# Optimization experiments

Measured on AMD Instinct MI355X. Metric: run time of the kernel, lower is better.

The kernel has to match this reference:

```python
import jax, jax.numpy as jnp
import numpy as np

GROUP = 128          # GPTQ quantization group size
H = 2048             # hidden_size
I = 1408             # moe_intermediate_size
T = 16384            # routed tokens


def _pack_rows(v):
    # v: [in, out] int4 values -> [in//8, out] int32 (8 nibbles per int32 along input dim)
    v = v.reshape(v.shape[0] // 8, 8, v.shape[1]).astype(jnp.int32)
    sh = (4 * jnp.arange(8, dtype=jnp.int32))[None, :, None]
    return (v << sh).sum(axis=1).astype(jnp.int32)


def _pack_cols(v):
    # v: [groups, out] int4 values -> [groups, out//8] int32
    v = v.reshape(v.shape[0], v.shape[1] // 8, 8).astype(jnp.int32)
    sh = (4 * jnp.arange(8, dtype=jnp.int32))[None, None, :]
    return (v << sh).sum(axis=-1).astype(jnp.int32)


def _unpack_rows(qw):
    # [in//8, out] int32 -> [in, out] int4 values
    sh = 4 * jnp.arange(8, dtype=jnp.int32)
    v = (qw[:, None, :] >> sh[None, :, None]) & 0xF
    return v.reshape(qw.shape[0] * 8, qw.shape[1])


def _unpack_cols(qz):
    # [groups, out//8] int32 -> [groups, out] int4 values
    sh = 4 * jnp.arange(8, dtype=jnp.int32)
    v = (qz[:, :, None] >> sh[None, None, :]) & 0xF
    return v.reshape(qz.shape[0], qz.shape[1] * 8)


def _dequant(qw, qz, sc):
    # GPTQ dequant: W[k, n] = (q[k, n] - (zero[g(k), n] + 1)) * scale[g(k), n]
    w = _unpack_rows(qw).astype(sc.dtype)                      # [in, out]
    z = (_unpack_cols(qz) + 1).astype(sc.dtype)                # [groups, out]
    scale = jnp.repeat(sc, GROUP, axis=0)                      # [in, out]
    zero = jnp.repeat(z, GROUP, axis=0)                        # [in, out]
    return (w - zero) * scale


def setup_inputs() -> dict:
    key = jax.random.key(0)
    ks = jax.random.split(key, 10)
    x = jax.random.normal(ks[0], (T, H), dtype=jnp.float32)

    def make_quant(kq, kz, ksc, n_in, n_out):
        q = jax.random.randint(kq, (n_in, n_out), 0, 16, dtype=jnp.int32)
        z = jax.random.randint(kz, (n_in // GROUP, n_out), 0, 15, dtype=jnp.int32)
        sc = jax.random.uniform(ksc, (n_in // GROUP, n_out), dtype=jnp.float32,
                                minval=1e-3, maxval=2e-2)
        return _pack_rows(q), _pack_cols(z), sc

    qw_g, qz_g, sc_g = make_quant(ks[1], ks[2], ks[3], H, I)
    qw_u, qz_u, sc_u = make_quant(ks[4], ks[5], ks[6], H, I)
    qw_d, qz_d, sc_d = make_quant(ks[7], ks[8], ks[9], I, H)
    return {"x": x,
            "qw_gate": qw_g, "qz_gate": qz_g, "sc_gate": sc_g,
            "qw_up": qw_u, "qz_up": qz_u, "sc_up": sc_u,
            "qw_down": qw_d, "qz_down": qz_d, "sc_down": sc_d}


def reference(x, qw_gate, qz_gate, sc_gate, qw_up, qz_up, sc_up,
              qw_down, qz_down, sc_down):
    Wg = _dequant(qw_gate, qz_gate, sc_gate)   # [H, I]
    Wu = _dequant(qw_up, qz_up, sc_up)         # [H, I]
    Wd = _dequant(qw_down, qz_down, sc_down)   # [I, H]
    # fused_gate_up: silu(x @ Wg) * (x @ Wu)
    h = jax.nn.silu(x @ Wg) * (x @ Wu)         # [T, I]
    return h @ Wd                              # [T, H]
```

## Files before the change

kernel.cpp:

```cpp
#include <hip/hip_runtime.h>

#define T_DIM 16384
#define H_DIM 2048
#define I_DIM 1408

typedef _Float16 half8 __attribute__((ext_vector_type(8)));
typedef float floatx4 __attribute__((ext_vector_type(4)));

static_assert(T_DIM % 128 == 0 && H_DIM % 128 == 0 && I_DIM % 128 == 0, "tile divisibility");

__device__ __forceinline__ void async_cp16(const _Float16* gp, _Float16* lp) {
    __builtin_amdgcn_global_load_lds(
        (const __attribute__((address_space(1))) unsigned int*)gp,
        (__attribute__((address_space(3))) unsigned int*)lp,
        16, 0, 0);
}

__global__ void cvt_fp16_kernel(const float* __restrict__ x, _Float16* __restrict__ xh) {
    int i = (blockIdx.x * 256 + threadIdx.x) * 8;
    const float4* p = (const float4*)(x + i);
    float4 a = p[0];
    float4 b = p[1];
    half8 o = { (_Float16)a.x, (_Float16)a.y, (_Float16)a.z, (_Float16)a.w,
                (_Float16)b.x, (_Float16)b.y, (_Float16)b.z, (_Float16)b.w };
    *(half8*)(xh + i) = o;
}

__global__ void dequant_kernel(const int* __restrict__ qw, const int* __restrict__ qz,
                               const float* __restrict__ sc, _Float16* __restrict__ Wt,
                               int K, int N) {
    int kp = blockIdx.x * 64 + threadIdx.x;
    int n  = blockIdx.y;
    if (kp >= (K >> 3)) return;
    int q = qw[kp * N + n];
    int g = kp >> 4;
    float scale = sc[g * N + n];
    int zq = (qz[g * (N >> 3) + (n >> 3)] >> (4 * (n & 7))) & 0xF;
    float zf = (float)(zq + 1);
    half8 o;
#pragma unroll
    for (int j = 0; j < 8; ++j) {
        float w = ((float)((q >> (4 * j)) & 0xF) - zf) * scale;
        o[j] = (_Float16)w;
    }
    *(half8*)(Wt + n * K + kp * 8) = o;
}

__launch_bounds__(256, 2)
__global__ void gemm_gateup_kernel(const _Float16* __restrict__ xh,
                                   const _Float16* __restrict__ Wg,
                                   const _Float16* __restrict__ Wu,
                                   _Float16* __restrict__ h) {
    __shared__ _Float16 As[128 * 32];
    __shared__ _Float16 Bgs[128 * 32];
    __shared__ _Float16 Bus[128 * 32];

    const int tid  = threadIdx.x;
    const int wave = tid >> 6;
    const int lane = tid & 63;
    const int m0 = blockIdx.y * 128;
    const int n0 = blockIdx.x * 128;
    const int wm = wave >> 1;
    const int wn = wave & 1;

    const int r0 = wave * 32 + (lane >> 2);
    const int ke = (lane & 3) * 8;
    const _Float16* agp0 = xh + (m0 + r0) * H_DIM + ke;
    const _Float16* agp1 = agp0 + 16 * H_DIM;
    const _Float16* bgp0 = Wg + (n0 + r0) * H_DIM + ke;
    const _Float16* bgp1 = bgp0 + 16 * H_DIM;
    const _Float16* bup0 = Wu + (n0 + r0) * H_DIM + ke;
    const _Float16* bup1 = bup0 + 16 * H_DIM;
    _Float16* lA0  = As  + wave * 1024;
    _Float16* lA1  = As  + wave * 1024 + 512;
    _Float16* lBg0 = Bgs + wave * 1024;
    _Float16* lBg1 = Bgs + wave * 1024 + 512;
    _Float16* lBu0 = Bus + wave * 1024;
    _Float16* lBu1 = Bus + wave * 1024 + 512;

    const int q4  = lane >> 4;
    const int l15 = lane & 15;
    const int a_base = (wm * 64 + l15) * 32 + q4 * 8;
    const int b_base = (wn * 64 + l15) * 32 + q4 * 8;

    floatx4 zero = {0.f, 0.f, 0.f, 0.f};
    floatx4 accg[4][4], accu[4][4];
#pragma unroll
    for (int mi = 0; mi < 4; ++mi)
#pragma unroll
        for (int ni = 0; ni < 4; ++ni) { accg[mi][ni] = zero; accu[mi][ni] = zero; }

    for (int kt = 0; kt < H_DIM; kt += 32) {
        __syncthreads();
        async_cp16(agp0 + kt, lA0);
        async_cp16(agp1 + kt, lA1);
        async_cp16(bgp0 + kt, lBg0);
        async_cp16(bgp1 + kt, lBg1);
        async_cp16(bup0 + kt, lBu0);
        async_cp16(bup1 + kt, lBu1);
        __syncthreads();

        half8 af[4], bgf[4], buf_[4];
#pragma unroll
        for (int mi = 0; mi < 4; ++mi)
            af[mi] = *(const half8*)(As + a_base + mi * 512);
#pragma unroll
        for (int ni = 0; ni < 4; ++ni) {
            bgf[ni]  = *(const half8*)(Bgs + b_base + ni * 512);
            buf_[ni] = *(const half8*)(Bus + b_base + ni * 512);
        }
#pragma unroll
        for (int mi = 0; mi < 4; ++mi)
#pragma unroll
            for (int ni = 0; ni < 4; ++ni) {
                accg[mi][ni] = __builtin_amdgcn_mfma_f32_16x16x32_f16(af[mi], bgf[ni], accg[mi][ni], 0, 0, 0);
                accu[mi][ni] = __builtin_amdgcn_mfma_f32_16x16x32_f16(af[mi], buf_[ni], accu[mi][ni], 0, 0, 0);
            }
    }

    const int rq = q4 * 4;
#pragma unroll
    for (int mi = 0; mi < 4; ++mi)
#pragma unroll
        for (int ni = 0; ni < 4; ++ni)
#pragma unroll
            for (int r = 0; r < 4; ++r) {
                int row = m0 + wm * 64 + mi * 16 + rq + r;
                int col = n0 + wn * 64 + ni * 16 + l15;
                float g = accg[mi][ni][r];
                float u = accu[mi][ni][r];
                float s = (g / (1.0f + __expf(-g))) * u;
                h[row * I_DIM + col] = (_Float16)s;
            }
}

__launch_bounds__(256, 2)
__global__ void gemm_down_kernel(const _Float16* __restrict__ hh,
                                 const _Float16* __restrict__ Wd,
                                 float* __restrict__ out) {
    __shared__ _Float16 As[128 * 32];
    __shared__ _Float16 Bs[128 * 32];

    const int tid  = threadIdx.x;
    const int wave = tid >> 6;
    const int lane = tid & 63;
    const int m0 = blockIdx.y * 128;
    const int n0 = blockIdx.x * 128;
    const int wm = wave >> 1;
    const int wn = wave & 1;

    const int r0 = wave * 32 + (lane >> 2);
    const int ke = (lane & 3) * 8;
    const _Float16* agp0 = hh + (m0 + r0) * I_DIM + ke;
    const _Float16* agp1 = agp0 + 16 * I_DIM;
    const _Float16* bgp0 = Wd + (n0 + r0) * I_DIM + ke;
    const _Float16* bgp1 = bgp0 + 16 * I_DIM;
    _Float16* lA0 = As + wave * 1024;
    _Float16* lA1 = As + wave * 1024 + 512;
    _Float16* lB0 = Bs + wave * 1024;
    _Float16* lB1 = Bs + wave * 1024 + 512;

    const int q4  = lane >> 4;
    const int l15 = lane & 15;
    const int a_base = (wm * 64 + l15) * 32 + q4 * 8;
    const int b_base = (wn * 64 + l15) * 32 + q4 * 8;

    floatx4 zero = {0.f, 0.f, 0.f, 0.f};
    floatx4 acc[4][4];
#pragma unroll
    for (int mi = 0; mi < 4; ++mi)
#pragma unroll
        for (int ni = 0; ni < 4; ++ni) acc[mi][ni] = zero;

    for (int kt = 0; kt < I_DIM; kt += 32) {
        __syncthreads();
        async_cp16(agp0 + kt, lA0);
        async_cp16(agp1 + kt, lA1);
        async_cp16(bgp0 + kt, lB0);
        async_cp16(bgp1 + kt, lB1);
        __syncthreads();

        half8 af[4], bf[4];
#pragma unroll
        for (int mi = 0; mi < 4; ++mi)
            af[mi] = *(const half8*)(As + a_base + mi * 512);
#pragma unroll
        for (int ni = 0; ni < 4; ++ni)
            bf[ni] = *(const half8*)(Bs + b_base + ni * 512);
#pragma unroll
        for (int mi = 0; mi < 4; ++mi)
#pragma unroll
            for (int ni = 0; ni < 4; ++ni)
                acc[mi][ni] = __builtin_amdgcn_mfma_f32_16x16x32_f16(af[mi], bf[ni], acc[mi][ni], 0, 0, 0);
    }

    const int rq = q4 * 4;
#pragma unroll
    for (int mi = 0; mi < 4; ++mi)
#pragma unroll
        for (int ni = 0; ni < 4; ++ni)
#pragma unroll
            for (int r = 0; r < 4; ++r) {
                int row = m0 + wm * 64 + mi * 16 + rq + r;
                int col = n0 + wn * 64 + ni * 16 + l15;
                out[row * H_DIM + col] = acc[mi][ni][r];
            }
}

extern "C" void kernel_launch(void* const* d_in, const int* in_sizes, int n_in,
                              void* d_out, int out_size, void* d_ws, size_t ws_size,
                              hipStream_t stream) {
    const float* x    = (const float*)d_in[0];
    const int* qw_g   = (const int*)d_in[1];
    const int* qz_g   = (const int*)d_in[2];
    const float* sc_g = (const float*)d_in[3];
    const int* qw_u   = (const int*)d_in[4];
    const int* qz_u   = (const int*)d_in[5];
    const float* sc_u = (const float*)d_in[6];
    const int* qw_d   = (const int*)d_in[7];
    const int* qz_d   = (const int*)d_in[8];
    const float* sc_d = (const float*)d_in[9];
    float* out = (float*)d_out;

    char* ws = (char*)d_ws;
    _Float16* xh = (_Float16*)ws;  ws += (size_t)T_DIM * H_DIM * sizeof(_Float16);
    _Float16* hh = (_Float16*)ws;  ws += (size_t)T_DIM * I_DIM * sizeof(_Float16);
    _Float16* Wg = (_Float16*)ws;  ws += (size_t)H_DIM * I_DIM * sizeof(_Float16);
    _Float16* Wu = (_Float16*)ws;  ws += (size_t)H_DIM * I_DIM * sizeof(_Float16);
    _Float16* Wd = (_Float16*)ws;  ws += (size_t)I_DIM * H_DIM * sizeof(_Float16);

    cvt_fp16_kernel<<<(T_DIM * H_DIM) / 2048, 256, 0, stream>>>(x, xh);
    dequant_kernel<<<dim3((H_DIM / 8 + 63) / 64, I_DIM), 64, 0, stream>>>(qw_g, qz_g, sc_g, Wg, H_DIM, I_DIM);
    dequant_kernel<<<dim3((H_DIM / 8 + 63) / 64, I_DIM), 64, 0, stream>>>(qw_u, qz_u, sc_u, Wu, H_DIM, I_DIM);
    dequant_kernel<<<dim3((I_DIM / 8 + 63) / 64, H_DIM), 64, 0, stream>>>(qw_d, qz_d, sc_d, Wd, I_DIM, H_DIM);
    gemm_gateup_kernel<<<dim3(I_DIM / 128, T_DIM / 128), 256, 0, stream>>>(xh, Wg, Wu, hh);
    gemm_down_kernel<<<dim3(H_DIM / 128, T_DIM / 128), 256, 0, stream>>>(hh, Wd, out);
}
```

Before: 595.8 us.

## Interleave gate/up weights into one B matrix and use XOR-swizzled K=64 tiles

Dequant now writes gate and up weights interleaved in 32-column chunks into a single [2I, H] matrix, using an LDS transpose so the global stores are coalesced. The gate-up GEMM becomes a plain 128x128 GEMM over this combined matrix, with gate in accumulator columns 0-1 and up in columns 2-3 of each wave. Both GEMMs move to K=64 tiles with an XOR-swizzled LDS layout to avoid bank conflicts, raise occupancy to 3 blocks per SM, and make blockIdx.x walk along M. The unused gemm_down kernel with a transposed accumulator index is left in the file but never launched.

```diff
diff --git a/kernel.cpp b/kernel.cpp
--- a/kernel.cpp
+++ b/kernel.cpp
@@ -3,11 +3,10 @@
 #define T_DIM 16384
 #define H_DIM 2048
 #define I_DIM 1408
+#define NB_DIM (2 * I_DIM)
 
 typedef _Float16 half8 __attribute__((ext_vector_type(8)));
 typedef float floatx4 __attribute__((ext_vector_type(4)));
-
-static_assert(T_DIM % 128 == 0 && H_DIM % 128 == 0 && I_DIM % 128 == 0, "tile divisibility");
 
 __device__ __forceinline__ void async_cp16(const _Float16* gp, _Float16* lp) {
     __builtin_amdgcn_global_load_lds(
@@ -28,10 +27,12 @@
 
 __global__ void dequant_kernel(const int* __restrict__ qw, const int* __restrict__ qz,
                                const float* __restrict__ sc, _Float16* __restrict__ Wt,
-                               int K, int N) {
-    int kp = blockIdx.x * 64 + threadIdx.x;
-    int n  = blockIdx.y;
-    if (kp >= (K >> 3)) return;
+                               int K, int N, int interleave, int off) {
+    __shared__ half8 tile[256];
+    int t = threadIdx.x;
+    int nl = t & 63, kl = t >> 6;
+    int n  = blockIdx.x * 64 + nl;
+    int kp = blockIdx.y * 4 + kl;
     int q = qw[kp * N + n];
     int g = kp >> 4;
     float scale = sc[g * N + n];
@@ -39,83 +40,149 @@
     float zf = (float)(zq + 1);
     half8 o;
 #pragma unroll
-    for (int j = 0; j < 8; ++j) {
-        float w = ((float)((q >> (4 * j)) & 0xF) - zf) * scale;
-        o[j] = (_Float16)w;
-    }
-    *(half8*)(Wt + n * K + kp * 8) = o;
-}
-
-__launch_bounds__(256, 2)
-__global__ void gemm_gateup_kernel(const _Float16* __restrict__ xh,
-                                   const _Float16* __restrict__ Wg,
-                                   const _Float16* __restrict__ Wu,
-                                   _Float16* __restrict__ h) {
-    __shared__ _Float16 As[128 * 32];
-    __shared__ _Float16 Bgs[128 * 32];
-    __shared__ _Float16 Bus[128 * 32];
-
-    const int tid  = threadIdx.x;
-    const int wave = tid >> 6;
-    const int lane = tid & 63;
-    const int m0 = blockIdx.y * 128;
-    const int n0 = blockIdx.x * 128;
-    const int wm = wave >> 1;
-    const int wn = wave & 1;
-
-    const int r0 = wave * 32 + (lane >> 2);
-    const int ke = (lane & 3) * 8;
-    const _Float16* agp0 = xh + (m0 + r0) * H_DIM + ke;
-    const _Float16* agp1 = agp0 + 16 * H_DIM;
-    const _Float16* bgp0 = Wg + (n0 + r0) * H_DIM + ke;
-    const _Float16* bgp1 = bgp0 + 16 * H_DIM;
-    const _Float16* bup0 = Wu + (n0 + r0) * H_DIM + ke;
-    const _Float16* bup1 = bup0 + 16 * H_DIM;
-    _Float16* lA0  = As  + wave * 1024;
-    _Float16* lA1  = As  + wave * 1024 + 512;
-    _Float16* lBg0 = Bgs + wave * 1024;
-    _Float16* lBg1 = Bgs + wave * 1024 + 512;
-    _Float16* lBu0 = Bus + wave * 1024;
-    _Float16* lBu1 = Bus + wave * 1024 + 512;
-
-    const int q4  = lane >> 4;
-    const int l15 = lane & 15;
-    const int a_base = (wm * 64 + l15) * 32 + q4 * 8;
-    const int b_base = (wn * 64 + l15) * 32 + q4 * 8;
+    for (int j = 0; j < 8; ++j)
+        o[j] = (_Float16)(((float)((q >> (4 * j)) & 0xF) - zf) * scale);
+    tile[nl * 4 + kl] = o;
+    __syncthreads();
+    int nl2 = t >> 2, kl2 = t & 3;
+    int n2 = blockIdx.x * 64 + nl2;
+    int np = interleave ? (((n2 >> 5) << 6) + (n2 & 31) + off) : n2;
+    *(half8*)(Wt + (size_t)np * K + (size_t)(blockIdx.y * 4 + kl2) * 8) = tile[nl2 * 4 + kl2];
+}
+
+
+__launch_bounds__(256, 3)
+__global__ void gemm_gateup(const _Float16* __restrict__ A,
+                            const _Float16* __restrict__ B,
+                            _Float16* __restrict__ h) {
+    __shared__ _Float16 As[128 * 64];
+    __shared__ _Float16 Bs[128 * 64];
+    const int t = threadIdx.x;
+    const int wave = t >> 6, lane = t & 63;
+    const int m0 = blockIdx.x * 128;
+    const int n0 = blockIdx.y * 128;
+    const int wm = wave >> 1, wn = wave & 1;
+
+    const int srow = wave * 8 + (lane >> 3);
+    const int schunk = (lane & 7) ^ (lane >> 3);
+    const _Float16* ag = A + (size_t)(m0 + srow) * H_DIM + schunk * 8;
+    const _Float16* bg = B + (size_t)(n0 + srow) * H_DIM + schunk * 8;
+    _Float16* lA = As + wave * 512;
+    _Float16* lB = Bs + wave * 512;
+
+    const int q4 = lane >> 4, l15 = lane & 15;
+    int aoff[4], boff[4];
+#pragma unroll
+    for (int i = 0; i < 4; ++i) {
+        int rA = wm * 64 + i * 16 + l15;
+        aoff[i] = rA * 64 + ((q4 ^ (rA & 7)) * 8);
+        int rB = wn * 64 + i * 16 + l15;
+        boff[i] = rB * 64 + ((q4 ^ (rB & 7)) * 8);
+    }
 
     floatx4 zero = {0.f, 0.f, 0.f, 0.f};
-    floatx4 accg[4][4], accu[4][4];
-#pragma unroll
-    for (int mi = 0; mi < 4; ++mi)
-#pragma unroll
-        for (int ni = 0; ni < 4; ++ni) { accg[mi][ni] = zero; accu[mi][ni] = zero; }
-
-    for (int kt = 0; kt < H_DIM; kt += 32) {
-        __syncthreads();
-        async_cp16(agp0 + kt, lA0);
-        async_cp16(agp1 + kt, lA1);
-        async_cp16(bgp0 + kt, lBg0);
-        async_cp16(bgp1 + kt, lBg1);
-        async_cp16(bup0 + kt, lBu0);
-        async_cp16(bup1 + kt, lBu1);
-        __syncthreads();
-
-        half8 af[4], bgf[4], buf_[4];
-#pragma unroll
-        for (int mi = 0; mi < 4; ++mi)
-            af[mi] = *(const half8*)(As + a_base + mi * 512);
-#pragma unroll
-        for (int ni = 0; ni < 4; ++ni) {
-            bgf[ni]  = *(const half8*)(Bgs + b_base + ni * 512);
-            buf_[ni] = *(const half8*)(Bus + b_base + ni * 512);
-        }
-#pragma unroll
-        for (int mi = 0; mi < 4; ++mi)
-#pragma unroll
-            for (int ni = 0; ni < 4; ++ni) {
-                accg[mi][ni] = __builtin_amdgcn_mfma_f32_16x16x32_f16(af[mi], bgf[ni], accg[mi][ni], 0, 0, 0);
-                accu[mi][ni] = __builtin_amdgcn_mfma_f32_16x16x32_f16(af[mi], buf_[ni], accu[mi][ni], 0, 0, 0);
+    floatx4 acc[4][4];
+#pragma unroll
+    for (int mi = 0; mi < 4; ++mi)
+#pragma unroll
+        for (int ni = 0; ni < 4; ++ni) acc[mi][ni] = zero;
+
+    for (int kt = 0; kt < H_DIM; kt += 64) {
+        __syncthreads();
+#pragma unroll
+        for (int i = 0; i < 4; ++i) {
+            async_cp16(ag + kt + (size_t)i * 32 * H_DIM, lA + i * 2048);
+            async_cp16(bg + kt + (size_t)i * 32 * H_DIM, lB + i * 2048);
+        }
+        __syncthreads();
+#pragma unroll
+        for (int kk = 0; kk < 2; ++kk) {
+            half8 af[4], bf[4];
+#pragma unroll
+            for (int i = 0; i < 4; ++i) af[i] = *(const half8*)(As + (aoff[i] ^ (kk * 32)));
+#pragma unroll
+            for (int i = 0; i < 4; ++i) bf[i] = *(const half8*)(Bs + (boff[i] ^ (kk * 32)));
+#pragma unroll
+            for (int mi = 0; mi < 4; ++mi)
+#pragma unroll
+                for (int ni = 0; ni < 4; ++ni)
+                    acc[mi][ni] = __builtin_amdgcn_mfma_f32_16x16x32_f16(af[mi], bf[ni], acc[mi][ni], 0, 0, 0);
+        }
+    }
+
+    const int rq = q4 * 4;
+#pragma unroll
+    for (int mi = 0; mi < 4; ++mi)
+#pragma unroll
+        for (int nc = 0; nc < 2; ++nc)
+#pragma unroll
+            for (int r = 0; r < 4; ++r) {
+                int row = m0 + wm * 64 + mi * 16 + rq + r;
+                int col = blockIdx.y * 64 + wn * 32 + nc * 16 + l15;
+                float g = acc[mi][nc][r];
+                float u = acc[mi][nc + 2][r];
+                float s = (g / (1.0f + __expf(-g))) * u;
+                h[(size_t)row * I_DIM + col] = (_Float16)s;
             }
+}
+
+__launch_bounds__(256, 3)
+__global__ void gemm_down(const _Float16* __restrict__ A,
+                          const _Float16* __restrict__ B,
+                          float* __restrict__ out) {
+    __shared__ _Float16 As[128 * 64];
+    __shared__ _Float16 Bs[128 * 64];
+    const int t = threadIdx.x;
+    const int wave = t >> 6, lane = t & 63;
+    const int m0 = blockIdx.x * 128;
+    const int n0 = blockIdx.y * 128;
+    const int wm = wave >> 1, wn = wave & 1;
+
+    const int srow = wave * 8 + (lane >> 3);
+    const int schunk = (lane & 7) ^ (lane >> 3);
+    const _Float16* ag = A + (size_t)(m0 + srow) * I_DIM + schunk * 8;
+    const _Float16* bg = B + (size_t)(n0 + srow) * I_DIM + schunk * 8;
+    _Float16* lA = As + wave * 512;
+    _Float16* lB = Bs + wave * 512;
+
+    const int q4 = lane >> 4, l15 = lane & 15;
+    int aoff[4], boff[4];
+#pragma unroll
+    for (int i = 0; i < 4; ++i) {
+        int rA = wm * 64 + i * 16 + l15;
+        aoff[i] = rA * 64 + ((q4 ^ (rA & 7)) * 8);
+        int rB = wn * 64 + i * 16 + l15;
+        boff[i] = rB * 64 + ((q4 ^ (rB & 7)) * 8);
+    }
+
+    floatx4 zero = {0.f, 0.f, 0.f, 0.f};
+    floatx4 acc[4][4];
+#pragma unroll
+    for (int mi = 0; mi < 4; ++mi)
+#pragma unroll
+        for (int ni = 0; ni < 4; ++ni) acc[mi][ni] = zero;
+
+    for (int kt = 0; kt < I_DIM; kt += 64) {
+        __syncthreads();
+#pragma unroll
+        for (int i = 0; i < 4; ++i) {
+            async_cp16(ag + kt + (size_t)i * 32 * I_DIM, lA + i * 2048);
+            async_cp16(bg + kt + (size_t)i * 32 * I_DIM, lB + i * 2048);
+        }
+        __syncthreads();
+#pragma unroll
+        for (int kk = 0; kk < 2; ++kk) {
+            half8 af[4], bf[4];
+#pragma unroll
+            for (int i = 0; i < 4; ++i) af[i] = *(const half8*)(As + (aoff[i] ^ (kk * 32)));
+#pragma unroll
+            for (int i = 0; i < 4; ++i) bf[i] = *(const half8*)(Bs + (boff[i] ^ (kk * 32)));
+#pragma unroll
+            for (int mi = 0; mi < 4; ++mi)
+#pragma unroll
+                for (int ni = 0; ni < 4; ++ni)
+                    acc[mi][ni] = __builtin_amdgcn_mfma_f32_16x16x32_f16(af[mi], bf[ni], acc[mi][ni], 0, 0, 0);
+        }
     }
 
     const int rq = q4 * 4;
@@ -127,43 +194,39 @@
             for (int r = 0; r < 4; ++r) {
                 int row = m0 + wm * 64 + mi * 16 + rq + r;
                 int col = n0 + wn * 64 + ni * 16 + l15;
-                float g = accg[mi][ni][r];
-                float u = accu[mi][ni][r];
-                float s = (g / (1.0f + __expf(-g))) * u;
-                h[row * I_DIM + col] = (_Float16)s;
+                out[(size_t)row * H_DIM + col] = acc[ni][mi][r];
             }
 }
 
-__launch_bounds__(256, 2)
-__global__ void gemm_down_kernel(const _Float16* __restrict__ hh,
-                                 const _Float16* __restrict__ Wd,
-                                 float* __restrict__ out) {
-    __shared__ _Float16 As[128 * 32];
-    __shared__ _Float16 Bs[128 * 32];
-
-    const int tid  = threadIdx.x;
-    const int wave = tid >> 6;
-    const int lane = tid & 63;
-    const int m0 = blockIdx.y * 128;
-    const int n0 = blockIdx.x * 128;
-    const int wm = wave >> 1;
-    const int wn = wave & 1;
-
-    const int r0 = wave * 32 + (lane >> 2);
-    const int ke = (lane & 3) * 8;
-    const _Float16* agp0 = hh + (m0 + r0) * I_DIM + ke;
-    const _Float16* agp1 = agp0 + 16 * I_DIM;
-    const _Float16* bgp0 = Wd + (n0 + r0) * I_DIM + ke;
-    const _Float16* bgp1 = bgp0 + 16 * I_DIM;
-    _Float16* lA0 = As + wave * 1024;
-    _Float16* lA1 = As + wave * 1024 + 512;
-    _Float16* lB0 = Bs + wave * 1024;
-    _Float16* lB1 = Bs + wave * 1024 + 512;
-
-    const int q4  = lane >> 4;
-    const int l15 = lane & 15;
-    const int a_base = (wm * 64 + l15) * 32 + q4 * 8;
-    const int b_base = (wn * 64 + l15) * 32 + q4 * 8;
+
+__launch_bounds__(256, 3)
+__global__ void gemm_down_fixed(const _Float16* __restrict__ A,
+                                const _Float16* __restrict__ B,
+                                float* __restrict__ out) {
+    __shared__ _Float16 As[128 * 64];
+    __shared__ _Float16 Bs[128 * 64];
+    const int t = threadIdx.x;
+    const int wave = t >> 6, lane = t & 63;
+    const int m0 = blockIdx.x * 128;
+    const int n0 = blockIdx.y * 128;
+    const int wm = wave >> 1, wn = wave & 1;
+
+    const int srow = wave * 8 + (lane >> 3);
+    const int schunk = (lane & 7) ^ (lane >> 3);
+    const _Float16* ag = A + (size_t)(m0 + srow) * I_DIM + schunk * 8;
+    const _Float16* bg = B + (size_t)(n0 + srow) * I_DIM + schunk * 8;
+    _Float16* lA = As + wave * 512;
+    _Float16* lB = Bs + wave * 512;
+
+    const int q4 = lane >> 4, l15 = lane & 15;
+    int aoff[4], boff[4];
+#pragma unroll
+    for (int i = 0; i < 4; ++i) {
+        int rA = wm * 64 + i * 16 + l15;
+        aoff[i] = rA * 64 + ((q4 ^ (rA & 7)) * 8);
+        int rB = wn * 64 + i * 16 + l15;
+        boff[i] = rB * 64 + ((q4 ^ (rB & 7)) * 8);
+    }
 
     floatx4 zero = {0.f, 0.f, 0.f, 0.f};
     floatx4 acc[4][4];
@@ -172,26 +235,27 @@
 #pragma unroll
         for (int ni = 0; ni < 4; ++ni) acc[mi][ni] = zero;
 
-    for (int kt = 0; kt < I_DIM; kt += 32) {
-        __syncthreads();
-        async_cp16(agp0 + kt, lA0);
-        async_cp16(agp1 + kt, lA1);
-        async_cp16(bgp0 + kt, lB0);
-        async_cp16(bgp1 + kt, lB1);
-        __syncthreads();
-
-        half8 af[4], bf[4];
-#pragma unroll
-        for (int mi = 0; mi < 4; ++mi)
-            af[mi] = *(const half8*)(As + a_base + mi * 512);
-#pragma unroll
-        for (int ni = 0; ni < 4; ++ni)
-            bf[ni] = *(const half8*)(Bs + b_base + ni * 512);
-#pragma unroll
-        for (int mi = 0; mi < 4; ++mi)
-#pragma unroll
-            for (int ni = 0; ni < 4; ++ni)
-                acc[mi][ni] = __builtin_amdgcn_mfma_f32_16x16x32_f16(af[mi], bf[ni], acc[mi][ni], 0, 0, 0);
+    for (int kt = 0; kt < I_DIM; kt += 64) {
+        __syncthreads();
+#pragma unroll
+        for (int i = 0; i < 4; ++i) {
+            async_cp16(ag + kt + (size_t)i * 32 * I_DIM, lA + i * 2048);
+            async_cp16(bg + kt + (size_t)i * 32 * I_DIM, lB + i * 2048);
+        }
+        __syncthreads();
+#pragma unroll
+        for (int kk = 0; kk < 2; ++kk) {
+            half8 af[4], bf[4];
+#pragma unroll
+            for (int i = 0; i < 4; ++i) af[i] = *(const half8*)(As + (aoff[i] ^ (kk * 32)));
+#pragma unroll
+            for (int i = 0; i < 4; ++i) bf[i] = *(const half8*)(Bs + (boff[i] ^ (kk * 32)));
+#pragma unroll
+            for (int mi = 0; mi < 4; ++mi)
+#pragma unroll
+                for (int ni = 0; ni < 4; ++ni)
+                    acc[mi][ni] = __builtin_amdgcn_mfma_f32_16x16x32_f16(af[mi], bf[ni], acc[mi][ni], 0, 0, 0);
+        }
     }
 
     const int rq = q4 * 4;
@@ -203,7 +267,7 @@
             for (int r = 0; r < 4; ++r) {
                 int row = m0 + wm * 64 + mi * 16 + rq + r;
                 int col = n0 + wn * 64 + ni * 16 + l15;
-                out[row * H_DIM + col] = acc[mi][ni][r];
+                out[(size_t)row * H_DIM + col] = acc[mi][ni][r];
             }
 }
 
@@ -223,16 +287,15 @@
     float* out = (float*)d_out;
 
     char* ws = (char*)d_ws;
-    _Float16* xh = (_Float16*)ws;  ws += (size_t)T_DIM * H_DIM * sizeof(_Float16);
-    _Float16* hh = (_Float16*)ws;  ws += (size_t)T_DIM * I_DIM * sizeof(_Float16);
-    _Float16* Wg = (_Float16*)ws;  ws += (size_t)H_DIM * I_DIM * sizeof(_Float16);
-    _Float16* Wu = (_Float16*)ws;  ws += (size_t)H_DIM * I_DIM * sizeof(_Float16);
-    _Float16* Wd = (_Float16*)ws;  ws += (size_t)I_DIM * H_DIM * sizeof(_Float16);
+    _Float16* xh  = (_Float16*)ws;  ws += (size_t)T_DIM * H_DIM * sizeof(_Float16);
+    _Float16* hh  = (_Float16*)ws;  ws += (size_t)T_DIM * I_DIM * sizeof(_Float16);
+    _Float16* Bgu = (_Float16*)ws;  ws += (size_t)NB_DIM * H_DIM * sizeof(_Float16);
+    _Float16* Wd  = (_Float16*)ws;  ws += (size_t)H_DIM * I_DIM * sizeof(_Float16);
 
     cvt_fp16_kernel<<<(T_DIM * H_DIM) / 2048, 256, 0, stream>>>(x, xh);
-    dequant_kernel<<<dim3((H_DIM / 8 + 63) / 64, I_DIM), 64, 0, stream>>>(qw_g, qz_g, sc_g, Wg, H_DIM, I_DIM);
-    dequant_kernel<<<dim3((H_DIM / 8 + 63) / 64, I_DIM), 64, 0, stream>>>(qw_u, qz_u, sc_u, Wu, H_DIM, I_DIM);
-    dequant_kernel<<<dim3((I_DIM / 8 + 63) / 64, H_DIM), 64, 0, stream>>>(qw_d, qz_d, sc_d, Wd, I_DIM, H_DIM);
-    gemm_gateup_kernel<<<dim3(I_DIM / 128, T_DIM / 128), 256, 0, stream>>>(xh, Wg, Wu, hh);
-    gemm_down_kernel<<<dim3(H_DIM / 128, T_DIM / 128), 256, 0, stream>>>(hh, Wd, out);
-}
+    dequant_kernel<<<dim3(I_DIM / 64, H_DIM / 32), 256, 0, stream>>>(qw_g, qz_g, sc_g, Bgu, H_DIM, I_DIM, 1, 0);
+    dequant_kernel<<<dim3(I_DIM / 64, H_DIM / 32), 256, 0, stream>>>(qw_u, qz_u, sc_u, Bgu, H_DIM, I_DIM, 1, 32);
+    dequant_kernel<<<dim3(H_DIM / 64, I_DIM / 32), 256, 0, stream>>>(qw_d, qz_d, sc_d, Wd, I_DIM, H_DIM, 0, 0);
+    gemm_gateup<<<dim3(T_DIM / 128, NB_DIM / 128), 256, 0, stream>>>(xh, Bgu, hh);
+    gemm_down_fixed<<<dim3(T_DIM / 128, H_DIM / 128), 256, 0, stream>>>(hh, Wd, out);
+}
```

Measured after the change: 518.1 us. -13.0%, faster.
